# Kernel optimization log

Hardware: AMD Instinct MI355X
Metric: run time of the kernel (lower is better)

## Reference

```python
import jax, jax.numpy as jnp
import numpy as np

B, C, H, W = 8, 6, 512, 512
N_SIGMA = 1
NUM_CLASS = 3
RES = 256
FG_W = 1.0
MAX_ID = 16  # instance ids in [0, 16); 0 is background
W_INST, W_VAR, W_SEED = 1.0, 10.0, 1.0
GAMMA = 2.0


def make_xym():
    ym = jnp.broadcast_to(jnp.linspace(0.0, H // RES, H)[None, :, None], (1, H, W))
    xm = jnp.broadcast_to(jnp.linspace(0.0, W // RES, W)[None, None, :], (1, H, W))
    return jnp.concatenate([xm, ym], 0)  # (2, H, W), channel 0 = x, 1 = y


def lovasz_hinge_flat(logits, labels_f):
    # logits, labels_f: (P,) ; labels in {0,1}
    signs = 2.0 * labels_f - 1.0
    errors = 1.0 - logits * signs
    order = jnp.argsort(-errors)  # descending
    errors_sorted = errors[order]
    gt_sorted = labels_f[order]
    gts = gt_sorted.sum()
    intersection = gts - jnp.cumsum(gt_sorted)
    union = gts + jnp.cumsum(1.0 - gt_sorted)
    jaccard = 1.0 - intersection / union
    grad = jaccard.at[1:].set(jaccard[1:] - jaccard[:-1])
    grad = jax.lax.stop_gradient(grad)
    return jnp.sum(jax.nn.relu(errors_sorted) * grad)


def focal_loss_multiclass(logits, target):
    # logits: (B, NUM_CLASS, H, W), target: (B, H, W) int class ids
    logpt = jax.nn.log_softmax(logits, axis=1)
    lp = jnp.take_along_axis(logpt, target[:, None], axis=1)[:, 0]  # (B,H,W)
    pt = jnp.exp(lp)
    return jnp.mean(-((1.0 - pt) ** GAMMA) * lp)


def setup_inputs() -> dict:
    key = jax.random.key(0)
    k1, k2, k3 = jax.random.split(key, 3)
    prediction = jax.random.normal(k1, (B, C, H, W), dtype=jnp.float32)
    labels = jax.random.randint(k2, (B, NUM_CLASS, H, W), 0, 2, dtype=jnp.int32)
    instances = jax.random.randint(k3, (B, 1, H, W), 0, MAX_ID, dtype=jnp.int32)
    return {"prediction": prediction, "labels": labels, "instances": instances}


def _loss(prediction, labels, instances):
    xym = make_xym()
    ids = jnp.arange(1, MAX_ID)

    def per_image(pred_b, inst_b, lab_b):
        spatial_emb = jnp.tanh(pred_b[0:2]) + xym           # (2,H,W)
        sigma = pred_b[2]                                    # (H,W), n_sigma=1
        seed = jax.nn.sigmoid(pred_b[2 + N_SIGMA + NUM_CLASS - 1])  # (H,W)
        label_fg = lab_b[-1]                                 # (H,W)
        bg_seed = jnp.sum(jnp.where(label_fg == 0, seed ** 2, 0.0))

        def per_id(k):
            mask = (inst_b[0] == k).astype(pred_b.dtype)     # (H,W)
            cnt = mask.sum()
            safe = jnp.maximum(cnt, 1.0)
            center = (xym * mask).sum((1, 2)) / safe         # (2,) to_center=True
            s_mean = (sigma * mask).sum() / safe
            var = (mask * (sigma - jax.lax.stop_gradient(s_mean)) ** 2).sum() / safe
            s = jnp.exp(s_mean * 10.0)
            dist = jnp.exp(-s * ((spatial_emb - center[:, None, None]) ** 2).sum(0))
            lov = lovasz_hinge_flat((dist * 2.0 - 1.0).ravel(), mask.ravel())
            seed_fg = FG_W * (mask * (seed - jax.lax.stop_gradient(dist)) ** 2).sum()
            return cnt > 0, lov, var, seed_fg

        valid, lov, var, sfg = jax.vmap(per_id)(ids)
        nobj = jnp.maximum(valid.sum().astype(pred_b.dtype), 1.0)
        inst_loss = jnp.where(valid, lov, 0.0).sum() / nobj
        var_loss = jnp.where(valid, var, 0.0).sum() / nobj
        seed_loss = (bg_seed + jnp.where(valid, sfg, 0.0).sum()) / (H * W)
        return W_INST * inst_loss + W_VAR * var_loss + W_SEED * seed_loss

    per_b = jax.vmap(per_image)(prediction, instances, labels)
    binary_closs = focal_loss_multiclass(
        prediction[:, 2 + N_SIGMA:2 + N_SIGMA + NUM_CLASS],
        jnp.argmax(labels, axis=1))
    return jnp.mean(per_b) + binary_closs


def reference(prediction, labels, instances):
    return _loss(prediction, labels, instances)
```

## Files before the change

### kernel.cpp

```cpp
#include <hip/hip_runtime.h>
#include <math.h>

#define BB 8
#define HWH (512*512)
#define NID 15
#define NSEG (BB*NID)
#define NBINS 256
#define AAF ((float)NBINS/13.0f)
#define LOG2E 1.442695041f
#define LN2 0.6931471806f
#define SLICES 128

typedef unsigned int uint32;
typedef unsigned long long uint64;

__device__ __forceinline__ float ftanh(float x){
    float t = __expf(2.0f*x);
    return 1.0f - 2.0f*__builtin_amdgcn_rcpf(t + 1.0f);
}
__device__ __forceinline__ float fsigmoid(float x){
    return __builtin_amdgcn_rcpf(1.0f + __expf(-x));
}
__device__ __forceinline__ float sconst(float x){
    return __uint_as_float(__builtin_amdgcn_readfirstlane(__float_as_uint(x)));
}

__global__ __launch_bounds__(256, 8) void phase1f(const float* __restrict__ pred,
        const int* __restrict__ labels, const int* __restrict__ inst,
        uint64* __restrict__ pstat64, float* __restrict__ pstatf,
        float* __restrict__ pstatf2,
        float* __restrict__ bgseed_p, float* __restrict__ focal_p){
    int blk = blockIdx.x;
    int b = blk >> 8;
    int t = threadIdx.x;
    int q = (blk & 255)*256 + t;

    __shared__ uint64 s64[NID];
    __shared__ float ssig[NID], ssig2[NID];
    __shared__ float wfb[4][2];
    if (t < NID){ s64[t] = 0ull; ssig[t] = 0.0f; ssig2[t] = 0.0f; }
    __syncthreads();

    const int Q = HWH/4;
    const float4* P = (const float4*)(pred + (size_t)b*6*HWH);
    const int4* L = (const int4*)(labels + (size_t)b*3*HWH);
    const int4* I = (const int4*)(inst + (size_t)b*HWH);
    float4 sg4 = P[2*Q+q], z3 = P[3*Q+q], z4 = P[4*Q+q], z5 = P[5*Q+q];
    int4 id4 = I[q];
    int4 l0 = L[q], l1 = L[Q+q], l2 = L[2*Q+q];
    int p = q*4;
    int w0 = p & 511, h0 = p >> 9;

    float facc = 0.0f, bacc = 0.0f;
    auto px = [&](float sgv, float z3v, float z4v, float z5v, int id,
                  int L0, int L1, int L2, int wv){
        float seed = fsigmoid(z5v);
        if (L2 == 0) bacc += seed*seed;
        int tc = 0, best = L0;
        if (L1 > best){ tc = 1; best = L1; }
        if (L2 > best){ tc = 2; }
        float m = fmaxf(z3v, fmaxf(z4v, z5v));
        float e3 = __expf(z3v-m), e4 = __expf(z4v-m), e5 = __expf(z5v-m);
        float sum = e3+e4+e5;
        float lse = m + __logf(sum);
        float zt = (tc==0) ? z3v : ((tc==1) ? z4v : z5v);
        float et = (tc==0) ? e3  : ((tc==1) ? e4  : e5);
        float lp = zt - lse;
        float pt = et*__builtin_amdgcn_rcpf(sum);
        float om = 1.0f - pt;
        facc -= om*om*lp;
        if (id > 0){
            atomicAdd(&s64[id-1],
                      (1ull<<42) | ((uint64)(uint32)wv<<21) | (uint64)(uint32)h0);
            atomicAdd(&ssig[id-1], sgv);
            atomicAdd(&ssig2[id-1], sgv*sgv);
        }
    };
    px(sg4.x, z3.x, z4.x, z5.x, id4.x, l0.x, l1.x, l2.x, w0);
    px(sg4.y, z3.y, z4.y, z5.y, id4.y, l0.y, l1.y, l2.y, w0+1);
    px(sg4.z, z3.z, z4.z, z5.z, id4.z, l0.z, l1.z, l2.z, w0+2);
    px(sg4.w, z3.w, z4.w, z5.w, id4.w, l0.w, l1.w, l2.w, w0+3);

    for (int o = 32; o; o >>= 1){
        facc += __shfl_xor(facc, o);
        bacc += __shfl_xor(bacc, o);
    }
    if ((t & 63) == 0){ wfb[t>>6][0] = facc; wfb[t>>6][1] = bacc; }
    __syncthreads();
    if (t < NID){
        pstat64[blk*16 + t] = s64[t];
        pstatf [blk*16 + t] = ssig[t];
        pstatf2[blk*16 + t] = ssig2[t];
    }
    if (t == 0){
        focal_p[blk]  = wfb[0][0]+wfb[1][0]+wfb[2][0]+wfb[3][0];
        bgseed_p[blk] = wfb[0][1]+wfb[1][1]+wfb[2][1]+wfb[3][1];
    }
}

__global__ __launch_bounds__(512) void phaseR(const uint64* __restrict__ pstat64,
        const float* __restrict__ pstatf, const float* __restrict__ pstatf2,
        const float* __restrict__ focal_p, const float* __restrict__ bgseed_p,
        float* __restrict__ stats, float* __restrict__ derived,
        float* __restrict__ results,
        float* __restrict__ focalR, float* __restrict__ bgseedR,
        uint32* __restrict__ Hzero, float* __restrict__ part2f){
    int b = blockIdx.x;
    int t = threadIdx.x;
    {
        const int stripe = 2*NSEG*NBINS/8;
        for (int i = b*stripe + t; i < (b+1)*stripe; i += 512) Hzero[i] = 0u;
        if (b == 0 && t < NSEG) part2f[t] = 0.0f;
    }
    int k = t & 15, chunk = t >> 4;
    float acnt = 0, asw = 0, ash = 0, af = 0, af2 = 0;
    for (int i = 0; i < 8; i++){
        int blk = b*256 + chunk*8 + i;
        uint64 v = pstat64[blk*16 + k];
        acnt += (float)(uint32)(v >> 42);
        asw  += (float)(uint32)((v >> 21) & 0x1FFFFF);
        ash  += (float)(uint32)(v & 0x1FFFFF);
        af   += pstatf[blk*16 + k];
        af2  += pstatf2[blk*16 + k];
    }
    __shared__ float tc[16], tw[16], th[16], ts[16], ts2[16];
    if (t < 16){ tc[t]=0; tw[t]=0; th[t]=0; ts[t]=0; ts2[t]=0; }
    __syncthreads();
    atomicAdd(&tc[k], acnt);
    atomicAdd(&tw[k], asw);
    atomicAdd(&th[k], ash);
    atomicAdd(&ts[k], af);
    atomicAdd(&ts2[k], af2);
    __syncthreads();
    if (t < NID){
        float cnt = tc[t];
        float safe = fmaxf(cnt, 1.0f);
        float inv = 1.0f/safe;
        const float SC = 2.0f/511.0f;
        derived[(b*NID+t)*4+0] = tw[t]*SC*inv;
        derived[(b*NID+t)*4+1] = th[t]*SC*inv;
        float sm = ts[t]*inv;
        derived[(b*NID+t)*4+2] = __expf(10.0f*sm);
        derived[(b*NID+t)*4+3] = sm;
        stats[b*60 + t*4] = cnt;
        results[(size_t)(b*NID+t)*3 + 1] = ts2[t] - cnt*sm*sm;
    }
    int w = t >> 6, lane = t & 63;
    if (w == 0){
        float f = 0;
        for (int j = 0; j < 4; j++) f += focal_p[b*256 + j*64 + lane];
        for (int o = 32; o; o >>= 1) f += __shfl_xor(f, o);
        if (lane == 0) focalR[b] = f;
    } else if (w == 1){
        float g = 0;
        for (int j = 0; j < 4; j++) g += bgseed_p[b*256 + j*64 + lane];
        for (int o = 32; o; o >>= 1) g += __shfl_xor(g, o);
        if (lane == 0) bgseedR[b] = g;
    }
}

__global__ __launch_bounds__(512, 8) void phaseLH(const float* __restrict__ pred,
        const int* __restrict__ inst, const float* __restrict__ derived,
        uint32* __restrict__ Hc, uint32* __restrict__ Hg,
        float* __restrict__ part2f){
    int idx = blockIdx.x;
    int b = idx & 7;
    int sp = idx >> 3;
    int t = threadIdx.x;

    __shared__ __align__(16) uint32 hist[NID*NBINS];
    __shared__ float ssl[NID];
    __shared__ float vsB[NID];
    {
        uint4* hz = (uint4*)hist;
        for (int i = t; i < NID*NBINS/4; i += 512) hz[i] = make_uint4(0,0,0,0);
    }
    if (t < NID){
        ssl[t] = derived[(size_t)(b*NID + t)*4 + 2];
        vsB[t] = 0.0f;
    }
    float kcx[NID], kcy[NID], kcs[NID];
    #pragma unroll
    for (int j = 0; j < NID; j++){
        const float* d0 = derived + (size_t)(b*NID + j)*4;
        kcx[j] = sconst(d0[0]);
        kcy[j] = sconst(d0[1]);
        kcs[j] = sconst(LOG2E*AAF*d0[2]);
    }
    __syncthreads();

    const int Q = HWH/4;
    const int qps = Q / SLICES;
    int q0 = sp * qps;
    const float* pb = pred + (size_t)b*6*HWH;
    const float4* P0 = (const float4*)pb;
    const float4* P1 = P0 + Q;
    const float* z5p = pb + 5*HWH;
    const int4* I = (const int4*)(inst + (size_t)b*HWH);
    const float SC = 2.0f/511.0f;

    for (int q = q0 + t; q < q0 + qps; q += 512){
        int4 id4 = I[q];
        float4 a = P0[q], c = P1[q];
        int p = q*4;
        float gx = (float)(p & 511)*SC;
        float gy = (float)(p >> 9)*SC;
        auto px = [&](float av, float cv, int id, float gxv, int pi){
            float ex = ftanh(av) + gxv;
            float ey = ftanh(cv) + gy;
            int own = id - 1;
            float r2own = 0.0f, binf_own = 0.0f;
            #pragma unroll
            for (int j = 0; j < NID; j++){
                float dx = ex - kcx[j], dy = ey - kcy[j];
                float r2 = fmaf(dx, dx, dy*dy);
                float binf = fmaf(-kcs[j], r2, (float)NBINS);
                binf = fminf(binf, (float)(NBINS-1));
                if (j == own){ r2own = r2; binf_own = binf; }
                if (binf >= 1.0f)
                    atomicAdd(&hist[j*NBINS + (int)binf], 65536u);
            }
            if (own >= 0){
                if (binf_own >= 1.0f)
                    atomicAdd(&hist[own*NBINS + (int)binf_own], 0xFFFF0000u);
                float s = ssl[own];
                float d = __expf(-s*r2own);
                float e = fmaf(-2.0f, d, 2.0f);
                float bf = fmaf(__log2f(e), AAF, (float)NBINS - AAF);
                bf = fminf(fmaxf(bf, 0.0f), (float)(NBINS-1));
                atomicAdd(&hist[own*NBINS + (int)bf], 65537u);
                float seed = fsigmoid(z5p[pi]);
                float sd = seed - d;
                atomicAdd(&vsB[own], sd*sd);
            }
        };
        px(a.x, c.x, id4.x, gx,      p);
        px(a.y, c.y, id4.y, gx+SC,   p+1);
        px(a.z, c.z, id4.z, gx+2*SC, p+2);
        px(a.w, c.w, id4.w, gx+3*SC, p+3);
    }
    __syncthreads();
    size_t base = (size_t)b*NID*NBINS;
    for (int i = t; i < NID*NBINS; i += 512){
        uint32 v = hist[i];
        if (v){
            uint32 cc = v >> 16, gg = v & 0xFFFFu;
            if (cc) atomicAdd(&Hc[base + i], cc);
            if (gg) atomicAdd(&Hg[base + i], gg);
        }
    }
    if (t < NID && vsB[t] != 0.0f)
        atomicAdd(&part2f[b*NID + t], vsB[t]);
}

__global__ __launch_bounds__(256) void phaseLS(const uint32* __restrict__ Hc,
        const uint32* __restrict__ Hg, const float* __restrict__ part2f,
        const float* __restrict__ stats, float* __restrict__ results){
    int idx = blockIdx.x;
    int b = idx & 7, k = idx >> 3;
    int seg = b*NID + k;
    int t = threadIdx.x;

    __shared__ uint32 wbc[4], wbg[4], wexc[4], wexg[4];
    __shared__ float wsum[4];

    size_t base = (size_t)seg*NBINS;
    uint32 cd = Hc[base + NBINS-1-t];
    uint32 gd = Hg[base + NBINS-1-t];
    uint32 ci = cd, gi2 = gd;
    int lane = t & 63, w = t >> 6;
    for (int o = 1; o < 64; o <<= 1){
        uint32 cu = __shfl_up(ci, o);
        uint32 gu = __shfl_up(gi2, o);
        if (lane >= o){ ci += cu; gi2 += gu; }
    }
    if (lane == 63){ wbc[w] = ci; wbg[w] = gi2; }
    __syncthreads();
    if (t == 0){
        uint32 rc = 0, rg = 0;
        for (int i = 0; i < 4; i++){
            uint32 a = wbc[i], bq = wbg[i];
            wexc[i] = rc; wexg[i] = rg;
            rc += a; rg += bq;
        }
    }
    __syncthreads();

    float G = stats[b*60 + k*4];
    uint32 cd_use = cd;
    if (t == NBINS-1){
        uint32 totalRaw = wexc[3] + wbc[3];
        cd_use = cd + ((uint32)HWH - totalRaw);
    }
    float contrib = 0.0f;
    if (G > 0.0f && (cd_use | gd)){
        uint32 nb = wexc[w] + (ci - cd);
        uint32 gb = wexg[w] + (gi2 - gd);
        float jp = 0.0f;
        if (nb > 0) jp = 1.0f - (G - (float)gb)/(G + (float)(nb - gb));
        uint32 n = nb + cd_use, gg = gb + gd;
        float j2 = 1.0f - (G - (float)gg)/(G + (float)(n - gg));
        int bin = NBINS-1-t;
        float ev = __expf(LN2*(((float)bin + 0.5f)*(13.0f/(float)NBINS) - 12.0f));
        contrib = ev*(j2 - jp);
    }
    for (int o = 32; o; o >>= 1) contrib += __shfl_xor(contrib, o);
    if (lane == 0) wsum[w] = contrib;
    __syncthreads();
    if (t == 0){
        results[(size_t)seg*3 + 0] = wsum[0]+wsum[1]+wsum[2]+wsum[3];
        results[(size_t)seg*3 + 2] = part2f[seg];
    }
}

__global__ void phase5(const float* __restrict__ stats, const float* __restrict__ results,
                       const float* __restrict__ bgseedR, const float* __restrict__ focalR,
                       float* __restrict__ out){
    int t = threadIdx.x;
    __shared__ float per_b[BB];
    if (t < BB){
        float nvalid = 0.0f, lsum = 0.0f, vsum = 0.0f, ssum = 0.0f;
        for (int k = 0; k < NID; k++){
            int seg = t*NID + k;
            float cnt = stats[t*60 + k*4];
            if (cnt > 0.0f){
                nvalid += 1.0f;
                lsum += results[(size_t)seg*3+0];
                vsum += results[(size_t)seg*3+1]/cnt;
                ssum += results[(size_t)seg*3+2];
            }
        }
        float nobj = fmaxf(nvalid, 1.0f);
        per_b[t] = lsum/nobj + 10.0f*(vsum/nobj) + (bgseedR[t] + ssum)/(float)HWH;
    }
    __syncthreads();
    if (t == 0){
        float s = 0.0f, fs = 0.0f;
        for (int b = 0; b < BB; b++){ s += per_b[b]; fs += focalR[b]; }
        out[0] = s/(float)BB + fs/(float)(BB*HWH);
    }
}

extern "C" void kernel_launch(void* const* d_in, const int* in_sizes, int n_in,
                              void* d_out, int out_size, void* d_ws, size_t ws_size,
                              hipStream_t stream){
    const float* pred  = (const float*)d_in[0];
    const int*   labels= (const int*)d_in[1];
    const int*   inst  = (const int*)d_in[2];
    float* out = (float*)d_out;

    uint32* Hc     = (uint32*)d_ws;
    uint32* Hg     = Hc + (size_t)NSEG*NBINS;
    float* part2f  = (float*)(Hg + (size_t)NSEG*NBINS);
    uint64* pstat64= (uint64*)(part2f + 128);
    float* pstatf  = (float*)(pstat64 + 2048*16);
    float* pstatf2 = pstatf + 2048*16;
    float* focal_p = pstatf2 + 2048*16;
    float* bgseed_p= focal_p + 2048;
    float* stats   = bgseed_p + 2048;
    float* derived = stats + 480;
    float* results = derived + 480;
    float* focalR  = results + 360;
    float* bgseedR = focalR + 8;

    hipLaunchKernelGGL(phase1f, dim3(2048), dim3(256), 0, stream,
                       pred, labels, inst, pstat64, pstatf, pstatf2,
                       bgseed_p, focal_p);
    hipLaunchKernelGGL(phaseR, dim3(8), dim3(512), 0, stream,
                       pstat64, pstatf, pstatf2, focal_p, bgseed_p,
                       stats, derived, results, focalR, bgseedR, Hc, part2f);
    hipLaunchKernelGGL(phaseLH, dim3(BB*SLICES), dim3(512), 0, stream,
                       pred, inst, derived, Hc, Hg, part2f);
    hipLaunchKernelGGL(phaseLS, dim3(NSEG), dim3(256), 0, stream,
                       Hc, Hg, part2f, stats, results);
    hipLaunchKernelGGL(phase5, dim3(1), dim3(64), 0, stream,
                       stats, results, bgseedR, focalR, out);
}
```

Before: 78.23 us.

## Fold final reduction into phaseLS atomics and move histogram zeroing into phase1f

Drops the single-block phase5 kernel. Each phaseLS block now adds its normalised segment contribution straight into the output with an atomicAdd, and phaseR adds the focal and background-seed terms the same way and records nobj per image. The zeroing of the histogram buffers and part2f moves from phaseR into phase1f, which already runs 2048 blocks, leaving phaseR with only 8 blocks of reduction work. The phaseLH loop becomes a single iteration with a remapped interleaved index, and the final sum now depends on float atomic ordering.

```diff
diff --git a/kernel.cpp b/kernel.cpp
--- a/kernel.cpp
+++ b/kernel.cpp
@@ -29,11 +29,17 @@
         const int* __restrict__ labels, const int* __restrict__ inst,
         uint64* __restrict__ pstat64, float* __restrict__ pstatf,
         float* __restrict__ pstatf2,
-        float* __restrict__ bgseed_p, float* __restrict__ focal_p){
+        float* __restrict__ bgseed_p, float* __restrict__ focal_p,
+        uint32* __restrict__ Hzero, float* __restrict__ part2f,
+        float* __restrict__ out){
     int blk = blockIdx.x;
     int b = blk >> 8;
     int t = threadIdx.x;
     int q = (blk & 255)*256 + t;
+
+    if (t < 30) Hzero[blk*30 + t] = 0u;
+    if (blk == 0 && t == 30) out[0] = 0.0f;
+    if (blk == 1 && t < NSEG) part2f[t] = 0.0f;
 
     __shared__ uint64 s64[NID];
     __shared__ float ssig[NID], ssig2[NID];
@@ -102,16 +108,10 @@
         const float* __restrict__ pstatf, const float* __restrict__ pstatf2,
         const float* __restrict__ focal_p, const float* __restrict__ bgseed_p,
         float* __restrict__ stats, float* __restrict__ derived,
-        float* __restrict__ results,
-        float* __restrict__ focalR, float* __restrict__ bgseedR,
-        uint32* __restrict__ Hzero, float* __restrict__ part2f){
+        float* __restrict__ results, float* __restrict__ nobjR,
+        float* __restrict__ out){
     int b = blockIdx.x;
     int t = threadIdx.x;
-    {
-        const int stripe = 2*NSEG*NBINS/8;
-        for (int i = b*stripe + t; i < (b+1)*stripe; i += 512) Hzero[i] = 0u;
-        if (b == 0 && t < NSEG) part2f[t] = 0.0f;
-    }
     int k = t & 15, chunk = t >> 4;
     float acnt = 0, asw = 0, ash = 0, af = 0, af2 = 0;
     for (int i = 0; i < 8; i++){
@@ -145,17 +145,22 @@
         stats[b*60 + t*4] = cnt;
         results[(size_t)(b*NID+t)*3 + 1] = ts2[t] - cnt*sm*sm;
     }
+    if (t == NID){
+        float nv = 0.0f;
+        for (int j = 0; j < NID; j++) nv += (tc[j] > 0.0f) ? 1.0f : 0.0f;
+        nobjR[b] = fmaxf(nv, 1.0f);
+    }
     int w = t >> 6, lane = t & 63;
     if (w == 0){
         float f = 0;
         for (int j = 0; j < 4; j++) f += focal_p[b*256 + j*64 + lane];
         for (int o = 32; o; o >>= 1) f += __shfl_xor(f, o);
-        if (lane == 0) focalR[b] = f;
+        if (lane == 0) atomicAdd(out, f/(float)(BB*HWH));
     } else if (w == 1){
         float g = 0;
         for (int j = 0; j < 4; j++) g += bgseed_p[b*256 + j*64 + lane];
         for (int o = 32; o; o >>= 1) g += __shfl_xor(g, o);
-        if (lane == 0) bgseedR[b] = g;
+        if (lane == 0) atomicAdd(out, g/(float)(BB*HWH));
     }
 }
 
@@ -167,6 +172,7 @@
     int b = idx & 7;
     int sp = idx >> 3;
     int t = threadIdx.x;
+    int lane = t & 63, w = t >> 6;
 
     __shared__ __align__(16) uint32 hist[NID*NBINS];
     __shared__ float ssl[NID];
@@ -199,7 +205,8 @@
     const int4* I = (const int4*)(inst + (size_t)b*HWH);
     const float SC = 2.0f/511.0f;
 
-    for (int q = q0 + t; q < q0 + qps; q += 512){
+    int q = q0 + lane*2 + (w & 1) + (w >> 1)*128;
+    {
         int4 id4 = I[q];
         float4 a = P0[q], c = P1[q];
         int p = q*4;
@@ -255,7 +262,8 @@
 
 __global__ __launch_bounds__(256) void phaseLS(const uint32* __restrict__ Hc,
         const uint32* __restrict__ Hg, const float* __restrict__ part2f,
-        const float* __restrict__ stats, float* __restrict__ results){
+        const float* __restrict__ stats, const float* __restrict__ results,
+        const float* __restrict__ nobjR, float* __restrict__ out){
     int idx = blockIdx.x;
     int b = idx & 7, k = idx >> 3;
     int seg = b*NID + k;
@@ -307,37 +315,14 @@
     for (int o = 32; o; o >>= 1) contrib += __shfl_xor(contrib, o);
     if (lane == 0) wsum[w] = contrib;
     __syncthreads();
-    if (t == 0){
-        results[(size_t)seg*3 + 0] = wsum[0]+wsum[1]+wsum[2]+wsum[3];
-        results[(size_t)seg*3 + 2] = part2f[seg];
-    }
-}
-
-__global__ void phase5(const float* __restrict__ stats, const float* __restrict__ results,
-                       const float* __restrict__ bgseedR, const float* __restrict__ focalR,
-                       float* __restrict__ out){
-    int t = threadIdx.x;
-    __shared__ float per_b[BB];
-    if (t < BB){
-        float nvalid = 0.0f, lsum = 0.0f, vsum = 0.0f, ssum = 0.0f;
-        for (int k = 0; k < NID; k++){
-            int seg = t*NID + k;
-            float cnt = stats[t*60 + k*4];
-            if (cnt > 0.0f){
-                nvalid += 1.0f;
-                lsum += results[(size_t)seg*3+0];
-                vsum += results[(size_t)seg*3+1]/cnt;
-                ssum += results[(size_t)seg*3+2];
-            }
-        }
-        float nobj = fmaxf(nvalid, 1.0f);
-        per_b[t] = lsum/nobj + 10.0f*(vsum/nobj) + (bgseedR[t] + ssum)/(float)HWH;
-    }
-    __syncthreads();
-    if (t == 0){
-        float s = 0.0f, fs = 0.0f;
-        for (int b = 0; b < BB; b++){ s += per_b[b]; fs += focalR[b]; }
-        out[0] = s/(float)BB + fs/(float)(BB*HWH);
+    if (t == 0 && G > 0.0f){
+        float lov = wsum[0]+wsum[1]+wsum[2]+wsum[3];
+        float nobj = nobjR[b];
+        float var = results[(size_t)seg*3 + 1];
+        float seedsum = part2f[seg];
+        float val = (lov + 10.0f*var/G)/(nobj*(float)BB)
+                  + seedsum/((float)HWH*(float)BB);
+        atomicAdd(out, val);
     }
 }
 
@@ -360,19 +345,16 @@
     float* stats   = bgseed_p + 2048;
     float* derived = stats + 480;
     float* results = derived + 480;
-    float* focalR  = results + 360;
-    float* bgseedR = focalR + 8;
+    float* nobjR   = results + 360;
 
     hipLaunchKernelGGL(phase1f, dim3(2048), dim3(256), 0, stream,
                        pred, labels, inst, pstat64, pstatf, pstatf2,
-                       bgseed_p, focal_p);
+                       bgseed_p, focal_p, Hc, part2f, out);
     hipLaunchKernelGGL(phaseR, dim3(8), dim3(512), 0, stream,
                        pstat64, pstatf, pstatf2, focal_p, bgseed_p,
-                       stats, derived, results, focalR, bgseedR, Hc, part2f);
+                       stats, derived, results, nobjR, out);
     hipLaunchKernelGGL(phaseLH, dim3(BB*SLICES), dim3(512), 0, stream,
                        pred, inst, derived, Hc, Hg, part2f);
     hipLaunchKernelGGL(phaseLS, dim3(NSEG), dim3(256), 0, stream,
-                       Hc, Hg, part2f, stats, results);
-    hipLaunchKernelGGL(phase5, dim3(1), dim3(64), 0, stream,
-                       stats, results, bgseedR, focalR, out);
-}
+                       Hc, Hg, part2f, stats, results, nobjR, out);
+}
```

New measurement: 74.88 us, median of 2. 4.3% less time.
